# Optimization experiments

Measured on AMD Instinct MI355X. Metric: run time of the kernel, lower is better.

## Reference

```python
import jax, jax.numpy as jnp
import numpy as np

# Config mirrors init_kwargs
H_FULL, W_FULL = 360, 720
SCALE = 4
H_LO, W_LO = H_FULL // SCALE, W_FULL // SCALE  # 90, 180
LMAX = H_LO                  # 90
MMAX = W_LO // 2 + 1         # 91
C = 128                      # embed_dim
NL = 4                       # num_layers
INP_CH, OUT_CH = 2, 2
MLP_HID = int(C * 2.0)
EPS = 1e-5


def rfft2_trunc(x):
    # RealFFT2.forward: ortho rfft2, keep first ceil(LMAX/2) and last floor(LMAX/2) lat modes, first MMAX lon modes
    y = jnp.fft.rfft2(x, norm="ortho")
    lt = (LMAX + 1) // 2
    lb = LMAX - lt
    return jnp.concatenate([y[..., :lt, :MMAX], y[..., y.shape[-2] - lb:, :MMAX]], axis=-2)


def irfft2_pad(y, H, W):
    # InverseRealFFT2: zero-pad truncated modes back to full spectrum, ortho irfft2
    lt = (LMAX + 1) // 2
    lb = LMAX - lt
    full = jnp.zeros(y.shape[:-2] + (H, W // 2 + 1), dtype=y.dtype)
    full = full.at[..., :lt, :MMAX].set(y[..., :lt, :])
    full = full.at[..., H - lb:, :MMAX].set(y[..., lt:, :])
    return jnp.fft.irfft2(full, s=(H, W), norm="ortho")


def inorm(x, w, b):
    # InstanceNorm2d(affine=True): per-sample, per-channel over spatial dims, biased var
    mu = x.mean(axis=(-2, -1), keepdims=True)
    var = x.var(axis=(-2, -1), keepdims=True)
    xn = (x - mu) * jax.lax.rsqrt(var + EPS)
    return xn * w[None, :, None, None] + b[None, :, None, None]


def conv1x1(x, w):  # w: [Cout, Cin], bias=False
    return jnp.einsum('bihw,oi->bohw', x, w)


def gelu(x):
    return jax.nn.gelu(x, approximate=False)


def fno_block(x, n0w, n0b, swr, swi, iw, n1w, n1b, mw1, mw2, out_hw):
    in_hw = x.shape[-2:]
    xn = inorm(x, n0w, n0b)
    # SpectralConv (dhconv): complex per-l channel mixing in truncated spectral space
    Xc = rfft2_trunc(xn)                                   # [B,C,LMAX,MMAX] complex
    scale_res = tuple(in_hw) != tuple(out_hw)
    residual = irfft2_pad(Xc, out_hw[0], out_hw[1]) if scale_res else xn
    w = swr + 1j * swi                                      # [Cin,Cout,LMAX]
    Yc = jnp.einsum('bilm,iol->bolm', Xc, w)
    h = irfft2_pad(Yc, out_hw[0], out_hw[1])
    h = h + conv1x1(residual, iw)                           # inner linear skip
    h = gelu(h)                                             # act_layer0
    h = inorm(h, n1w, n1b)                                  # norm1
    h = conv1x1(gelu(conv1x1(h, mw1)), mw2)                 # MLP (1x1 convs)
    return h + residual                                     # outer identity skip


def setup_inputs() -> dict:
    key = jax.random.key(0)
    ks = jax.random.split(key, 16)
    s = 1.0 / np.sqrt(C)
    inp = {
        "x": jax.random.normal(ks[0], (1, INP_CH, H_FULL, W_FULL), jnp.float32),
        # encoder: inp_chans -> C -> C (encoder_ratio=1)
        "enc_w1": jax.random.normal(ks[1], (C, INP_CH), jnp.float32) * (1.0 / np.sqrt(INP_CH)),
        "enc_w2": jax.random.normal(ks[2], (C, C), jnp.float32) * s,
        # per-layer stacked block params
        "n0w": jnp.ones((NL, C), jnp.float32),
        "n0b": jnp.zeros((NL, C), jnp.float32),
        "swr": jax.random.normal(ks[3], (NL, C, C, LMAX), jnp.float32) * (1.0 / C),
        "swi": jax.random.normal(ks[4], (NL, C, C, LMAX), jnp.float32) * (1.0 / C),
        "iw": jax.random.normal(ks[5], (NL, C, C), jnp.float32) * s,
        "n1w": jnp.ones((NL, C), jnp.float32),
        "n1b": jnp.zeros((NL, C), jnp.float32),
        "mw1": jax.random.normal(ks[6], (NL, MLP_HID, C), jnp.float32) * s,
        "mw2": jax.random.normal(ks[7], (NL, C, MLP_HID), jnp.float32) * (1.0 / np.sqrt(MLP_HID)),
        # decoder: (C + inp_chans) -> C -> out_chans (big_skip concat)
        "dec_w1": jax.random.normal(ks[8], (C, C + INP_CH), jnp.float32) * (1.0 / np.sqrt(C + INP_CH)),
        "dec_w2": jax.random.normal(ks[9], (OUT_CH, C), jnp.float32) * s,
    }
    return inp


def reference(x, enc_w1, enc_w2, n0w, n0b, swr, swi, iw, n1w, n1b, mw1, mw2, dec_w1, dec_w2):
    big_res = x
    h = conv1x1(gelu(conv1x1(x, enc_w1)), enc_w2)           # encoder
    out_shapes = [(H_LO, W_LO)] * (NL - 1) + [(H_FULL, W_FULL)]
    for l in range(NL):
        h = fno_block(h, n0w[l], n0b[l], swr[l], swi[l], iw[l],
                      n1w[l], n1b[l], mw1[l], mw2[l], out_shapes[l])
    h = jnp.concatenate([h, big_res], axis=1)               # big skip
    h = conv1x1(gelu(conv1x1(h, dec_w1)), dec_w2)           # decoder
    return h
```

## Files before the change

### kernel.cpp

```cpp
#include <hip/hip_runtime.h>
#include <hip/hip_bf16.h>
#include <math.h>

typedef __attribute__((ext_vector_type(8))) short short8v;
typedef __attribute__((ext_vector_type(4))) float f32x4;
typedef unsigned short u16;

__device__ __forceinline__ float gelu_f(float x) {
    return 0.5f * x * (1.0f + erff(x * 0.70710678118654752f));
}
__device__ __forceinline__ float bf2f(u16 u) {
    union { unsigned int i; float f; } v; v.i = ((unsigned int)u) << 16; return v.f;
}
__device__ __forceinline__ u16 f2bf(float f) {
    union { float f; unsigned int i; } v; v.f = f;
    unsigned int r = v.i + 0x7FFFu + ((v.i >> 16) & 1u);
    return (u16)(r >> 16);
}

__device__ __forceinline__ uint4 load8(const u16* p) { return *(const uint4*)p; }
__device__ __forceinline__ uint4 load8(const float* p) {
    float4 a = *(const float4*)p;
    float4 b = *(const float4*)(p + 4);
    union { uint4 u; u16 e[8]; } r;
    r.e[0] = f2bf(a.x); r.e[1] = f2bf(a.y); r.e[2] = f2bf(a.z); r.e[3] = f2bf(a.w);
    r.e[4] = f2bf(b.x); r.e[5] = f2bf(b.y); r.e[6] = f2bf(b.z); r.e[7] = f2bf(b.w);
    return r.u;
}
__device__ __forceinline__ float rdD(const u16* p) { return bf2f(*p); }
__device__ __forceinline__ float rdD(const float* p) { return *p; }
__device__ __forceinline__ void stO(u16* p, float v) { *p = f2bf(v); }
__device__ __forceinline__ void stO(float* p, float v) { *p = v; }

template<int BMODE, class TA, class TB, class TD, class TO>
__global__ __launch_bounds__(256) void gemm_t(
    const TA* __restrict__ A1, const TB* __restrict__ B1,
    const TA* __restrict__ A2, const TB* __restrict__ B2,
    const TD* __restrict__ D, TO* __restrict__ O,
    int M, int N, int Kp, int neg2, int act,
    long long sAb, long long sAm,
    long long sBb, long long sBr,
    long long sDb, long long sDm,
    long long sOb, long long sOm)
{
    __shared__ __align__(16) u16 As[64 * 32];
    __shared__ __align__(16) u16 Bs[BMODE ? 32 * 68 : 64 * 32];
    const int tid = threadIdx.x;
    const long long b = blockIdx.z;
    const int bm0 = blockIdx.y * 64;
    const int bn0 = blockIdx.x * 64;
    const int lane = tid & 63;
    const int wave = tid >> 6;
    const int wr = (wave >> 1) * 32;
    const int wc = (wave & 1) * 32;
    const int fr = lane & 15;
    const int fg = lane >> 4;
    const int arow = tid >> 2, achk = tid & 3;

    f32x4 acc[2][2];
#pragma unroll
    for (int i = 0; i < 2; ++i)
#pragma unroll
        for (int j = 0; j < 2; ++j) acc[i][j] = (f32x4){0.f, 0.f, 0.f, 0.f};

    const int nph = A2 ? 2 : 1;
    for (int ph = 0; ph < nph; ++ph) {
        const TA* Ap = (ph ? A2 : A1) + b * sAb;
        const TB* Bp = (ph ? B2 : B1) + b * sBb;
        const unsigned int sgn = (ph && neg2) ? 0x80008000u : 0u;
        for (int k0 = 0; k0 < Kp; k0 += 32) {
            uint4 av = load8(Ap + (long long)(bm0 + arow) * sAm + k0 + achk * 8);
            av.x ^= sgn; av.y ^= sgn; av.z ^= sgn; av.w ^= sgn;
            uint4 bv;
            if (BMODE == 0) {
                bv = load8(Bp + (long long)(bn0 + arow) * sBr + k0 + achk * 8);
            } else {
                const int bk = tid >> 3, bnc = tid & 7;
                bv = load8(Bp + (long long)(k0 + bk) * sBr + bn0 + bnc * 8);
            }
            __syncthreads();
            *(uint4*)(&As[arow * 32 + ((achk ^ ((arow >> 1) & 3)) * 8)]) = av;
            if (BMODE == 0) {
                *(uint4*)(&Bs[arow * 32 + ((achk ^ ((arow >> 1) & 3)) * 8)]) = bv;
            } else {
                const int bk = tid >> 3, bnc = tid & 7;
                *(uint2*)(&Bs[bk * 68 + bnc * 8]) = make_uint2(bv.x, bv.y);
                *(uint2*)(&Bs[bk * 68 + bnc * 8 + 4]) = make_uint2(bv.z, bv.w);
            }
            __syncthreads();
            short8v afrag[2], bfrag[2];
#pragma unroll
            for (int i = 0; i < 2; ++i) {
                int r = wr + i * 16 + fr;
                afrag[i] = *(const short8v*)(&As[r * 32 + ((fg ^ ((r >> 1) & 3)) * 8)]);
            }
            if (BMODE == 0) {
#pragma unroll
                for (int j = 0; j < 2; ++j) {
                    int r = wc + j * 16 + fr;
                    bfrag[j] = *(const short8v*)(&Bs[r * 32 + ((fg ^ ((r >> 1) & 3)) * 8)]);
                }
            } else {
#pragma unroll
                for (int j = 0; j < 2; ++j) {
                    int col = wc + j * 16 + fr;
                    short8v v;
#pragma unroll
                    for (int e = 0; e < 8; ++e) v[e] = (short)Bs[(fg * 8 + e) * 68 + col];
                    bfrag[j] = v;
                }
            }
#pragma unroll
            for (int i = 0; i < 2; ++i)
#pragma unroll
                for (int j = 0; j < 2; ++j)
                    acc[i][j] = __builtin_amdgcn_mfma_f32_16x16x32_bf16(afrag[i], bfrag[j], acc[i][j], 0, 0, 0);
        }
    }
#pragma unroll
    for (int i = 0; i < 2; ++i) {
#pragma unroll
        for (int j = 0; j < 2; ++j) {
            int col = bn0 + wc + j * 16 + fr;
            if (col >= N) continue;
#pragma unroll
            for (int r = 0; r < 4; ++r) {
                int row = bm0 + wr + i * 16 + fg * 4 + r;
                if (row >= M) continue;
                float v = acc[i][j][r];
                if (D) v += rdD(D + b * sDb + (long long)row * sDm + col);
                if (act) v = gelu_f(v);
                stO(O + b * sOb + (long long)row * sOm + col, v);
            }
        }
    }
}

__global__ void gen_fwdW_T(u16* Cm, u16* Sm, int RP, int KP, int W, int MM) {
    int idx = blockIdx.x * blockDim.x + threadIdx.x;
    if (idx >= RP * KP) return;
    int m = idx / KP, w = idx % KP;
    float cv = 0.f, sv = 0.f;
    if (m < MM && w < W) {
        int t = (m * w) % W;
        float arg = 2.0f * (float)t / (float)W;
        float s = 1.0f / sqrtf((float)W);
        cv = cospif(arg) * s; sv = -sinpif(arg) * s;
    }
    Cm[idx] = f2bf(cv); Sm[idx] = f2bf(sv);
}
__global__ void gen_fwdH(u16* Cm, u16* Sm, int RP, int KP, int H) {
    int idx = blockIdx.x * blockDim.x + threadIdx.x;
    if (idx >= RP * KP) return;
    int l = idx / KP, h = idx % KP;
    float cv = 0.f, sv = 0.f;
    if (l < 90 && h < H) {
        int ll = (l < 45) ? l : l + H - 90;
        int t = (ll * h) % H;
        float arg = 2.0f * (float)t / (float)H;
        float s = 1.0f / sqrtf((float)H);
        cv = cospif(arg) * s; sv = sinpif(arg) * s;
    }
    Cm[idx] = f2bf(cv); Sm[idx] = f2bf(sv);
}
__global__ void gen_invH(u16* Cm, u16* Sm, int RP, int KP, int H) {
    int idx = blockIdx.x * blockDim.x + threadIdx.x;
    if (idx >= RP * KP) return;
    int y = idx / KP, l = idx % KP;
    float cv = 0.f, sv = 0.f;
    if (y < H && l < 90) {
        int ll = (l < 45) ? l : l + H - 90;
        int t = (ll * y) % H;
        float arg = 2.0f * (float)t / (float)H;
        float s = 1.0f / sqrtf((float)H);
        cv = cospif(arg) * s; sv = sinpif(arg) * s;
    }
    Cm[idx] = f2bf(cv); Sm[idx] = f2bf(sv);
}
__global__ void gen_invW_T(u16* Cm, u16* Sm, int RP, int KP, int W, int MM) {
    int idx = blockIdx.x * blockDim.x + threadIdx.x;
    if (idx >= RP * KP) return;
    int w = idx / KP, m = idx % KP;
    float cv = 0.f, sv = 0.f;
    if (w < W && m < MM) {
        int t = (m * w) % W;
        float arg = 2.0f * (float)t / (float)W;
        bool nyq = (2 * m == W);
        float wt = (m == 0 || nyq) ? 1.0f : 2.0f;
        float s = wt / sqrtf((float)W);
        cv = cospif(arg) * s;
        sv = nyq ? 0.f : sinpif(arg) * s;
    }
    Cm[idx] = f2bf(cv); Sm[idx] = f2bf(sv);
}

__global__ void w2bf(const float* __restrict__ in, u16* __restrict__ out, int R, int K, int rs) {
    int idx = blockIdx.x * blockDim.x + threadIdx.x;
    if (idx >= R * K) return;
    int r = idx / K, c = idx % K;
    out[idx] = f2bf(in[(long long)r * rs + c]);
}
__global__ void transp_sw(const float* __restrict__ in, u16* __restrict__ out) {
    __shared__ float t[32][33];
    int l0 = blockIdx.x * 32, ci0 = blockIdx.y * 32, co = blockIdx.z;
    int tx = threadIdx.x, ty = threadIdx.y;
#pragma unroll
    for (int rr = 0; rr < 4; ++rr) {
        int ci = ci0 + ty + rr * 8;
        int l = l0 + tx;
        t[ty + rr * 8][tx] = (l < 90) ? in[((long long)ci * 128 + co) * 90 + l] : 0.f;
    }
    __syncthreads();
#pragma unroll
    for (int rr = 0; rr < 4; ++rr) {
        int l = l0 + ty + rr * 8;
        int ci = ci0 + tx;
        if (l < 90) out[((long long)l * 128 + co) * 128 + ci] = f2bf(t[tx][ty + rr * 8]);
    }
}

__global__ __launch_bounds__(256) void stats_cl_bf(const u16* __restrict__ x, long long P,
                                                   float2* __restrict__ part, int nch) {
    int chunk = blockIdx.x;
    int c = threadIdx.x & 127;
    int h = threadIdx.x >> 7;
    long long beg = P * chunk / nch, end = P * (chunk + 1) / nch;
    float s = 0.f, q = 0.f;
    long long p = beg + h;
    for (; p + 14 < end; p += 16) {
        float v[8];
#pragma unroll
        for (int u = 0; u < 8; ++u) v[u] = bf2f(x[(p + 2 * u) * 128 + c]);
#pragma unroll
        for (int u = 0; u < 8; ++u) { s += v[u]; q += v[u] * v[u]; }
    }
    for (; p < end; p += 2) {
        float v = bf2f(x[p * 128 + c]);
        s += v; q += v * v;
    }
    __shared__ float rs[256], rq[256];
    rs[threadIdx.x] = s; rq[threadIdx.x] = q;
    __syncthreads();
    if (threadIdx.x < 128)
        part[(long long)c * nch + chunk] = make_float2(rs[c] + rs[c + 128], rq[c] + rq[c + 128]);
}
__global__ __launch_bounds__(256) void stats_cl_f32(const float* __restrict__ x, long long P,
                                                    float2* __restrict__ part, int nch) {
    int chunk = blockIdx.x;
    long long beg = P * chunk / nch, end = P * (chunk + 1) / nch;
    int c32 = threadIdx.x & 31;
    int pr  = threadIdx.x >> 5;
    float s[4], q[4];
#pragma unroll
    for (int k = 0; k < 4; ++k) { s[k] = 0.f; q[k] = 0.f; }
    for (long long p = beg + pr; p < end; p += 8) {
        float4 v = *(const float4*)(x + p * 128 + c32 * 4);
        float e[4] = {v.x, v.y, v.z, v.w};
#pragma unroll
        for (int k = 0; k < 4; ++k) { s[k] += e[k]; q[k] += e[k] * e[k]; }
    }
#pragma unroll
    for (int k = 0; k < 4; ++k) {
        s[k] += __shfl_xor(s[k], 32); q[k] += __shfl_xor(q[k], 32);
    }
    __shared__ float2 lds[4][128];
    int wv = threadIdx.x >> 6, lane = threadIdx.x & 63;
    if (lane < 32) {
#pragma unroll
        for (int k = 0; k < 4; ++k) lds[wv][lane * 4 + k] = make_float2(s[k], q[k]);
    }
    __syncthreads();
    if (threadIdx.x < 128) {
        float2 a = lds[0][threadIdx.x], b2 = lds[1][threadIdx.x];
        float2 c2 = lds[2][threadIdx.x], d2 = lds[3][threadIdx.x];
        part[(long long)threadIdx.x * nch + chunk] =
            make_float2(a.x + b2.x + c2.x + d2.x, a.y + b2.y + c2.y + d2.y);
    }
}
__global__ void stats_fin(const float2* __restrict__ part, int nch, float Pf,
                          const float* __restrict__ w, const float* __restrict__ b,
                          float2* __restrict__ st) {
    int c = threadIdx.x;
    float s = 0.f, q = 0.f;
    for (int i = 0; i < nch; ++i) { float2 p = part[(long long)c * nch + i]; s += p.x; q += p.y; }
    float mu = s / Pf;
    float var = q / Pf - mu * mu;
    float inv = rsqrtf(var + 1e-5f);
    float sc = w[c] * inv;
    st[c] = make_float2(sc, b[c] - mu * sc);
}
__global__ __launch_bounds__(256) void norm_apply_bf(const u16* __restrict__ src, u16* __restrict__ dst,
                                                     long long n8, const float2* __restrict__ st) {
    long long i = (long long)blockIdx.x * 256 + threadIdx.x;
    if (i >= n8) return;
    int c0 = (int)((i * 8) & 127);
    uint4 v = *(const uint4*)(src + i * 8);
    union { uint4 u; u16 e[8]; } in, out;
    in.u = v;
#pragma unroll
    for (int k = 0; k < 8; ++k) {
        float2 s = st[c0 + k];
        out.e[k] = f2bf(bf2f(in.e[k]) * s.x + s.y);
    }
    *(uint4*)(dst + i * 8) = out.u;
}
__global__ __launch_bounds__(256) void norm_apply_f32(const float4* __restrict__ src, float4* __restrict__ dst,
                                                      long long n4, const float2* __restrict__ st) {
    long long i = (long long)blockIdx.x * 256 + threadIdx.x;
    if (i >= n4) return;
    int c0 = (int)((i * 4) & 127);
    float4 v = src[i];
    float2 s0 = st[c0], s1 = st[c0 + 1], s2 = st[c0 + 2], s3 = st[c0 + 3];
    v.x = v.x * s0.x + s0.y;
    v.y = v.y * s1.x + s1.y;
    v.z = v.z * s2.x + s2.y;
    v.w = v.w * s3.x + s3.y;
    dst[i] = v;
}

__global__ __launch_bounds__(256) void enc_front(const float* __restrict__ x, const float* __restrict__ w1,
                                                 u16* __restrict__ out, long long P) {
    long long idx = (long long)blockIdx.x * 256 + threadIdx.x;
    if (idx >= P * 16) return;
    long long p = idx >> 4;
    int c0 = (int)(idx & 15) * 8;
    float x0 = x[p], x1 = x[P + p];
    union { uint4 u; u16 e[8]; } o;
#pragma unroll
    for (int k = 0; k < 8; ++k) {
        int c = c0 + k;
        o.e[k] = f2bf(gelu_f(w1[c * 2] * x0 + w1[c * 2 + 1] * x1));
    }
    *(uint4*)(out + p * 128 + c0) = o.u;
}
__global__ __launch_bounds__(256) void dec_mid(u16* __restrict__ s, const float* __restrict__ dw1,
                                               const float* __restrict__ x, long long P) {
    long long idx = (long long)blockIdx.x * 256 + threadIdx.x;
    if (idx >= P * 16) return;
    long long p = idx >> 4;
    int c0 = (int)(idx & 15) * 8;
    float x0 = x[p], x1 = x[P + p];
    union { uint4 u; u16 e[8]; } io;
    io.u = *(const uint4*)(s + p * 128 + c0);
#pragma unroll
    for (int k = 0; k < 8; ++k) {
        int c = c0 + k;
        io.e[k] = f2bf(gelu_f(bf2f(io.e[k]) + dw1[c * 130 + 128] * x0 + dw1[c * 130 + 129] * x1));
    }
    *(uint4*)(s + p * 128 + c0) = io.u;
}
__global__ __launch_bounds__(256) void dec_back(const u16* __restrict__ d1, const float* __restrict__ w2,
                                                float* __restrict__ out, long long P) {
    __shared__ float w2s[256];
    w2s[threadIdx.x] = w2[threadIdx.x];
    __syncthreads();
    int lane = threadIdx.x & 63;
    long long pix = (long long)blockIdx.x * 4 + (threadIdx.x >> 6);
    unsigned int pr = *(const unsigned int*)(d1 + pix * 128 + lane * 2);
    float b0 = bf2f((u16)(pr & 0xFFFF)), b1 = bf2f((u16)(pr >> 16));
    float s0 = b0 * w2s[lane * 2] + b1 * w2s[lane * 2 + 1];
    float s1 = b0 * w2s[128 + lane * 2] + b1 * w2s[128 + lane * 2 + 1];
#pragma unroll
    for (int off = 1; off < 64; off <<= 1) {
        s0 += __shfl_xor(s0, off);
        s1 += __shfl_xor(s1, off);
    }
    if (lane == 0) { out[pix] = s0; out[P + pix] = s1; }
}

__global__ void zero_out(float* p, long long n) {
    long long i = (long long)blockIdx.x * 256 + threadIdx.x;
    if (i < n) p[i] = 0.f;
}

extern "C" void kernel_launch(void* const* d_in, const int* in_sizes, int n_in,
                              void* d_out, int out_size, void* d_ws, size_t ws_size,
                              hipStream_t stream)
{
    const int HF = 360, WF = 720, HL = 90, WL = 180, C = 128, MM = 91;
    const long long PF = (long long)HF * WF;
    const long long PL = (long long)HL * WL;
    (void)in_sizes; (void)n_in;

    const float* x      = (const float*)d_in[0];
    const float* enc_w1 = (const float*)d_in[1];
    const float* enc_w2 = (const float*)d_in[2];
    const float* n0w    = (const float*)d_in[3];
    const float* n0b    = (const float*)d_in[4];
    const float* swr    = (const float*)d_in[5];
    const float* swi    = (const float*)d_in[6];
    const float* iw     = (const float*)d_in[7];
    const float* n1w    = (const float*)d_in[8];
    const float* n1b    = (const float*)d_in[9];
    const float* mw1    = (const float*)d_in[10];
    const float* mw2    = (const float*)d_in[11];
    const float* dec_w1 = (const float*)d_in[12];
    const float* dec_w2 = (const float*)d_in[13];
    float* outp = (float*)d_out;

    u16* ws = (u16*)d_ws;
    long long off = 0;
    auto alloc = [&](long long n) { u16* p = ws + off; off += (n + 31) & ~31LL; return p; };
    auto allocF = [&](long long n) { return (float*)alloc(2 * n); };

    u16*   FULL = alloc(PF * C);
    u16*   RES  = alloc(PF * C);
    u16*   S1r  = alloc(96LL * 384 * 128);
    u16*   S1i  = alloc(96LL * 384 * 128);
    float* Xr   = allocF(96LL * 96 * 128);
    float* Xi   = allocF(96LL * 96 * 128);
    float* Yr   = allocF(96LL * 96 * 128);
    float* Yi   = allocF(96LL * 96 * 128);
    u16*   G1r  = alloc(360LL * 96 * 128);
    u16*   G1i  = alloc(360LL * 96 * 128);
    u16*   G3r  = alloc(360LL * 96 * 128);
    u16*   G3i  = alloc(360LL * 96 * 128);
    float* Rlo  = allocF(PL * C);
    float* L0   = allocF(PL * C);
    u16*   HID  = alloc(43200LL * 256);
    u16*   WtR  = alloc(90LL * 128 * 128);
    u16*   WtI  = alloc(90LL * 128 * 128);
    u16* encw2b = alloc(128 * 128);
    u16* iwb    = alloc(128 * 128);
    u16* m1b    = alloc(256 * 128);
    u16* m2b    = alloc(128 * 256);
    u16* dw1b   = alloc(128 * 128);
    u16* CwTc_h = alloc(128 * 736); u16* CwTs_h = alloc(128 * 736);
    u16* CwTc_l = alloc(128 * 192); u16* CwTs_l = alloc(128 * 192);
    u16* Chc_h  = alloc(128 * 384); u16* Chs_h  = alloc(128 * 384);
    u16* Chc_l  = alloc(128 * 96);  u16* Chs_l  = alloc(128 * 96);
    u16* C2c_h  = alloc(384 * 96);  u16* C2s_h  = alloc(384 * 96);
    u16* C2c_l  = alloc(128 * 96);  u16* C2s_l  = alloc(128 * 96);
    u16* CwIc_h = alloc(768 * 96);  u16* CwIs_h = alloc(768 * 96);
    u16* CwIc_l = alloc(192 * 96);  u16* CwIs_l = alloc(192 * 96);
    float2* PART = (float2*)alloc(128 * 256 * 4);
    float2* STb  = (float2*)alloc(128 * 4);
    alloc(64 * 1024);

    if ((size_t)(off * 2) > ws_size) {
        zero_out<<<(int)((out_size + 255) / 256), 256, 0, stream>>>(outp, out_size);
        return;
    }

    auto grid3 = [](int M, int N, int batch) {
        return dim3((unsigned)((N + 63) / 64), (unsigned)((M + 63) / 64), (unsigned)batch);
    };
    auto inormB = [&](const u16* src, u16* dst, long long P, int nch,
                      const float* w, const float* b) {
        stats_cl_bf<<<nch, 256, 0, stream>>>(src, P, PART, nch);
        stats_fin<<<1, 128, 0, stream>>>(PART, nch, (float)P, w, b, STb);
        long long n8 = P * 128 / 8;
        norm_apply_bf<<<(int)((n8 + 255) / 256), 256, 0, stream>>>(src, dst, n8, STb);
    };
    auto inormF = [&](const float* src, float* dst, long long P, int nch,
                      const float* w, const float* b) {
        stats_cl_f32<<<nch, 256, 0, stream>>>(src, P, PART, nch);
        stats_fin<<<1, 128, 0, stream>>>(PART, nch, (float)P, w, b, STb);
        long long n4 = P * 128 / 4;
        norm_apply_f32<<<(int)((n4 + 255) / 256), 256, 0, stream>>>(
            (const float4*)src, (float4*)dst, n4, STb);
    };

    const u16* nullU = nullptr;
    const float* nullF = nullptr;

    {
        int n;
        n = 128 * 736; gen_fwdW_T<<<(n + 255) / 256, 256, 0, stream>>>(CwTc_h, CwTs_h, 128, 736, 720, MM);
        n = 128 * 192; gen_fwdW_T<<<(n + 255) / 256, 256, 0, stream>>>(CwTc_l, CwTs_l, 128, 192, 180, MM);
        n = 128 * 384; gen_fwdH<<<(n + 255) / 256, 256, 0, stream>>>(Chc_h, Chs_h, 128, 384, 360);
        n = 128 * 96;  gen_fwdH<<<(n + 255) / 256, 256, 0, stream>>>(Chc_l, Chs_l, 128, 96, 90);
        n = 384 * 96;  gen_invH<<<(n + 255) / 256, 256, 0, stream>>>(C2c_h, C2s_h, 384, 96, 360);
        n = 128 * 96;  gen_invH<<<(n + 255) / 256, 256, 0, stream>>>(C2c_l, C2s_l, 128, 96, 90);
        n = 768 * 96;  gen_invW_T<<<(n + 255) / 256, 256, 0, stream>>>(CwIc_h, CwIs_h, 768, 96, 720, MM);
        n = 192 * 96;  gen_invW_T<<<(n + 255) / 256, 256, 0, stream>>>(CwIc_l, CwIs_l, 192, 96, 180, MM);
        n = 128 * 128; w2bf<<<(n + 255) / 256, 256, 0, stream>>>(enc_w2, encw2b, 128, 128, 128);
        n = 128 * 128; w2bf<<<(n + 255) / 256, 256, 0, stream>>>(dec_w1, dw1b, 128, 128, 130);
    }

    enc_front<<<(int)((PF * 16 + 255) / 256), 256, 0, stream>>>(x, enc_w1, RES, PF);
    gemm_t<0, u16, u16, u16, u16><<<grid3((int)PF, 128, 1), 256, 0, stream>>>(
        RES, encw2b, nullU, nullU, nullU, FULL, (int)PF, 128, 128, 0, 0,
        0, 128, 0, 128, 0, 0, 0, 128);

    const long long s96 = 96LL * 128;

    for (int l = 0; l < 4; ++l) {
        const bool inHi = (l == 0), outHi = (l == 3);
        const int Hin = inHi ? HF : HL, Win = inHi ? WF : WL;
        const int Hout = outHi ? HF : HL, Wout = outHi ? WF : WL;
        const long long Pout = (long long)Hout * Wout;
        const int hdim = inHi ? 384 : 96;
        const int Wp = inHi ? 736 : 192;
        const int hp = inHi ? 384 : 96;
        const u16* CwTc = inHi ? CwTc_h : CwTc_l;  const u16* CwTs = inHi ? CwTs_h : CwTs_l;
        const u16* Chc  = inHi ? Chc_h  : Chc_l;   const u16* Chs  = inHi ? Chs_h  : Chs_l;
        const u16* C2c  = outHi ? C2c_h : C2c_l;   const u16* C2s  = outHi ? C2s_h : C2s_l;
        const u16* CwIc = outHi ? CwIc_h : CwIc_l; const u16* CwIs = outHi ? CwIs_h : CwIs_l;

        {
            dim3 gt(3, 4, 128); dim3 bt(32, 8);
            transp_sw<<<gt, bt, 0, stream>>>(swr + (long long)l * C * C * 90, WtR);
            transp_sw<<<gt, bt, 0, stream>>>(swi + (long long)l * C * C * 90, WtI);
            int n = 128 * 128; w2bf<<<(n + 255) / 256, 256, 0, stream>>>(iw + (long long)l * C * C, iwb, 128, 128, 128);
            n = 256 * 128; w2bf<<<(n + 255) / 256, 256, 0, stream>>>(mw1 + (long long)l * 256 * C, m1b, 256, 128, 128);
            n = 128 * 256; w2bf<<<(n + 255) / 256, 256, 0, stream>>>(mw2 + (long long)l * C * 256, m2b, 128, 256, 256);
        }

        if (inHi) {
            inormB(FULL, RES, PF, 256, n0w + l * C, n0b + l * C);
            gemm_t<1, u16, u16, u16, u16><<<grid3(96, 128, Hin), 256, 0, stream>>>(
                CwTc, RES, nullU, nullU, nullU, S1r, 96, 128, Wp, 0, 0,
                0, Wp, (long long)Win * 128, 128, 0, 0, 128, (long long)hdim * 128);
            gemm_t<1, u16, u16, u16, u16><<<grid3(96, 128, Hin), 256, 0, stream>>>(
                CwTs, RES, nullU, nullU, nullU, S1i, 96, 128, Wp, 0, 0,
                0, Wp, (long long)Win * 128, 128, 0, 0, 128, (long long)hdim * 128);
        } else {
            inormF(Rlo, L0, PL, 128, n0w + l * C, n0b + l * C);
            gemm_t<1, u16, float, u16, u16><<<grid3(96, 128, Hin), 256, 0, stream>>>(
                CwTc, L0, nullU, nullF, nullU, S1r, 96, 128, Wp, 0, 0,
                0, Wp, (long long)Win * 128, 128, 0, 0, 128, (long long)hdim * 128);
            gemm_t<1, u16, float, u16, u16><<<grid3(96, 128, Hin), 256, 0, stream>>>(
                CwTs, L0, nullU, nullF, nullU, S1i, 96, 128, Wp, 0, 0,
                0, Wp, (long long)Win * 128, 128, 0, 0, 128, (long long)hdim * 128);
        }

        gemm_t<1, u16, u16, u16, float><<<grid3(96, 128, 96), 256, 0, stream>>>(
            Chc, S1r, Chs, S1i, nullU, Xr, 96, 128, hp, 0, 0,
            0, hp, (long long)hdim * 128, 128, 0, 0, 128, s96);
        gemm_t<1, u16, u16, u16, float><<<grid3(96, 128, 96), 256, 0, stream>>>(
            Chc, S1i, Chs, S1r, nullU, Xi, 96, 128, hp, 1, 0,
            0, hp, (long long)hdim * 128, 128, 0, 0, 128, s96);

        if (inHi || outHi) {
            gemm_t<1, u16, float, u16, u16><<<grid3(Hout, 128, 96), 256, 0, stream>>>(
                C2c, Xr, C2s, Xi, nullU, G3r, Hout, 128, 96, 1, 0,
                0, 96, 128, s96, 0, 0, 128, s96);
            gemm_t<1, u16, float, u16, u16><<<grid3(Hout, 128, 96), 256, 0, stream>>>(
                C2c, Xi, C2s, Xr, nullU, G3i, Hout, 128, 96, 0, 0,
                0, 96, 128, s96, 0, 0, 128, s96);
        }

        gemm_t<0, float, u16, u16, float><<<grid3(96, 128, 90), 256, 0, stream>>>(
            Xr, WtR, Xi, WtI, nullU, Yr, 96, 128, 128, 1, 0,
            s96, 128, 128LL * 128, 128, 0, 0, 128, s96);
        gemm_t<0, float, u16, u16, float><<<grid3(96, 128, 90), 256, 0, stream>>>(
            Xr, WtI, Xi, WtR, nullU, Yi, 96, 128, 128, 0, 0,
            s96, 128, 128LL * 128, 128, 0, 0, 128, s96);

        gemm_t<1, u16, float, u16, u16><<<grid3(Hout, 128, 96), 256, 0, stream>>>(
            C2c, Yr, C2s, Yi, nullU, G1r, Hout, 128, 96, 1, 0,
            0, 96, s96, 128, 0, 0, 128, s96);
        gemm_t<1, u16, float, u16, u16><<<grid3(Hout, 128, 96), 256, 0, stream>>>(
            C2c, Yi, C2s, Yr, nullU, G1i, Hout, 128, 96, 0, 0,
            0, 96, s96, 128, 0, 0, 128, s96);

        if (!outHi) {
            gemm_t<1, u16, u16, u16, float><<<grid3(Wout, 128, Hout), 256, 0, stream>>>(
                CwIc, G1r, CwIs, G1i, nullU, Rlo, Wout, 128, 96, 1, 0,
                0, 96, s96, 128, 0, 0, (long long)Wout * 128, 128);
            if (inHi)
                gemm_t<1, u16, u16, u16, float><<<grid3(Wout, 128, Hout), 256, 0, stream>>>(
                    CwIc, G3r, CwIs, G3i, nullU, L0, Wout, 128, 96, 1, 0,
                    0, 96, s96, 128, 0, 0, (long long)Wout * 128, 128);
            gemm_t<0, float, u16, float, float><<<grid3((int)Pout, 128, 1), 256, 0, stream>>>(
                L0, iwb, nullF, nullU, Rlo, Rlo, (int)Pout, 128, 128, 0, 1,
                0, 128, 0, 128, 0, 128, 0, 128);
            inormF(Rlo, Rlo, Pout, 128, n1w + l * C, n1b + l * C);
            gemm_t<0, float, u16, u16, u16><<<grid3((int)Pout, 256, 1), 256, 0, stream>>>(
                Rlo, m1b, nullF, nullU, nullU, HID, (int)Pout, 256, 128, 0, 1,
                0, 128, 0, 128, 0, 0, 0, 256);
            gemm_t<0, u16, u16, float, float><<<grid3((int)Pout, 128, 1), 256, 0, stream>>>(
                HID, m2b, nullU, nullU, L0, Rlo, (int)Pout, 128, 256, 0, 0,
                0, 256, 0, 256, 0, 128, 0, 128);
        } else {
            gemm_t<1, u16, u16, u16, u16><<<grid3(Wout, 128, Hout), 256, 0, stream>>>(
                CwIc, G1r, CwIs, G1i, nullU, FULL, Wout, 128, 96, 1, 0,
                0, 96, s96, 128, 0, 0, (long long)Wout * 128, 128);
            gemm_t<1, u16, u16, u16, u16><<<grid3(Wout, 128, Hout), 256, 0, stream>>>(
                CwIc, G3r, CwIs, G3i, nullU, RES, Wout, 128, 96, 1, 0,
                0, 96, s96, 128, 0, 0, (long long)Wout * 128, 128);
            gemm_t<0, u16, u16, u16, u16><<<grid3((int)Pout, 128, 1), 256, 0, stream>>>(
                RES, iwb, nullU, nullU, FULL, FULL, (int)Pout, 128, 128, 0, 1,
                0, 128, 0, 128, 0, 128, 0, 128);
            inormB(FULL, FULL, Pout, 256, n1w + l * C, n1b + l * C);
            const int nchunk = 6;
            const long long chM = Pout / nchunk;
            for (int ch = 0; ch < nchunk; ++ch) {
                long long o2 = ch * chM * 128;
                gemm_t<0, u16, u16, u16, u16><<<grid3((int)chM, 256, 1), 256, 0, stream>>>(
                    FULL + o2, m1b, nullU, nullU, nullU, HID, (int)chM, 256, 128, 0, 1,
                    0, 128, 0, 128, 0, 0, 0, 256);
                gemm_t<0, u16, u16, u16, u16><<<grid3((int)chM, 128, 1), 256, 0, stream>>>(
                    HID, m2b, nullU, nullU, RES + o2, FULL + o2, (int)chM, 128, 256, 0, 0,
                    0, 256, 0, 256, 0, 128, 0, 128);
            }
        }
    }

    gemm_t<0, u16, u16, u16, u16><<<grid3((int)PF, 128, 1), 256, 0, stream>>>(
        FULL, dw1b, nullU, nullU, nullU, RES, (int)PF, 128, 128, 0, 0,
        0, 128, 0, 128, 0, 0, 0, 128);
    dec_mid<<<(int)((PF * 16 + 255) / 256), 256, 0, stream>>>(RES, dec_w1, x, PF);
    dec_back<<<(int)(PF / 4), 256, 0, stream>>>(RES, dec_w2, outp, PF);
}
```

Measured before the change: 1.440 ms.

## Fuse real/imaginary GEMM pairs into a single complex-GEMM kernel

Adds a gemm_t2 kernel that computes both output planes of a complex matrix product in one launch, loading the shared operand tiles once and applying sign flips by XOR on bf16 fragments. It replaces the paired real/imag launches for the forward DFT, the per-mode channel mixing and the inverse latitude DFT. The aim is to halve launches and global operand reads. In exchange each block holds twice the accumulators and more shared memory, which may lower occupancy.

```diff
diff --git a/kernel.cpp b/kernel.cpp
--- a/kernel.cpp
+++ b/kernel.cpp
@@ -16,6 +16,11 @@
     union { float f; unsigned int i; } v; v.f = f;
     unsigned int r = v.i + 0x7FFFu + ((v.i >> 16) & 1u);
     return (u16)(r >> 16);
+}
+__device__ __forceinline__ short8v negbf(short8v a) {
+    uint4 u = *(uint4*)&a;
+    u.x ^= 0x80008000u; u.y ^= 0x80008000u; u.z ^= 0x80008000u; u.w ^= 0x80008000u;
+    return *(short8v*)&u;
 }
 
 __device__ __forceinline__ uint4 load8(const u16* p) { return *(const uint4*)p; }
@@ -131,6 +136,151 @@
                 if (D) v += rdD(D + b * sDb + (long long)row * sDm + col);
                 if (act) v = gelu_f(v);
                 stO(O + b * sOb + (long long)row * sOm + col, v);
+            }
+        }
+    }
+}
+
+template<int BMODE, int MODE, class TA, class TB, class TO>
+__global__ __launch_bounds__(256) void gemm_t2(
+    const TA* __restrict__ A1, const TA* __restrict__ A2,
+    const TB* __restrict__ B1, const TB* __restrict__ B2,
+    TO* __restrict__ O1, TO* __restrict__ O2,
+    int M, int N, int Kp, int s2neg,
+    long long sAb, long long sAm,
+    long long sBb, long long sBr,
+    long long sOb, long long sOm)
+{
+    __shared__ __align__(16) u16 As1[64 * 32], As2[64 * 32];
+    __shared__ __align__(16) u16 Bs1[BMODE ? 32 * 68 : 64 * 32];
+    __shared__ __align__(16) u16 Bs2[(MODE == 1) ? 16 : (BMODE ? 32 * 68 : 64 * 32)];
+    const int tid = threadIdx.x;
+    const long long b = blockIdx.z;
+    const int bm0 = blockIdx.y * 64;
+    const int bn0 = blockIdx.x * 64;
+    const int lane = tid & 63;
+    const int wave = tid >> 6;
+    const int wr = (wave >> 1) * 32;
+    const int wc = (wave & 1) * 32;
+    const int fr = lane & 15;
+    const int fg = lane >> 4;
+    const int arow = tid >> 2, achk = tid & 3;
+    const int aswz = (achk ^ ((arow >> 1) & 3)) * 8;
+
+    f32x4 acc1[2][2], acc2[2][2];
+#pragma unroll
+    for (int i = 0; i < 2; ++i)
+#pragma unroll
+        for (int j = 0; j < 2; ++j) {
+            acc1[i][j] = (f32x4){0.f, 0.f, 0.f, 0.f};
+            acc2[i][j] = (f32x4){0.f, 0.f, 0.f, 0.f};
+        }
+
+    const TA* A1b = A1 + b * sAb;
+    const TA* A2b = A2 + b * sAb;
+    const TB* B1b = B1 + b * sBb;
+    const TB* B2b = (MODE == 0) ? B2 + b * sBb : B1;
+
+    for (int k0 = 0; k0 < Kp; k0 += 32) {
+        long long aoff = (long long)(bm0 + arow) * sAm + k0 + achk * 8;
+        uint4 av1 = load8(A1b + aoff);
+        uint4 av2 = load8(A2b + aoff);
+        uint4 bv1, bv2;
+        if (BMODE == 0) {
+            long long boff = (long long)(bn0 + arow) * sBr + k0 + achk * 8;
+            bv1 = load8(B1b + boff);
+            if (MODE == 0) bv2 = load8(B2b + boff);
+        } else {
+            const int bk = tid >> 3, bnc = tid & 7;
+            long long boff = (long long)(k0 + bk) * sBr + bn0 + bnc * 8;
+            bv1 = load8(B1b + boff);
+            if (MODE == 0) bv2 = load8(B2b + boff);
+        }
+        __syncthreads();
+        *(uint4*)(&As1[arow * 32 + aswz]) = av1;
+        *(uint4*)(&As2[arow * 32 + aswz]) = av2;
+        if (BMODE == 0) {
+            *(uint4*)(&Bs1[arow * 32 + aswz]) = bv1;
+            if (MODE == 0) *(uint4*)(&Bs2[arow * 32 + aswz]) = bv2;
+        } else {
+            const int bk = tid >> 3, bnc = tid & 7;
+            *(uint2*)(&Bs1[bk * 68 + bnc * 8]) = make_uint2(bv1.x, bv1.y);
+            *(uint2*)(&Bs1[bk * 68 + bnc * 8 + 4]) = make_uint2(bv1.z, bv1.w);
+            if (MODE == 0) {
+                *(uint2*)(&Bs2[bk * 68 + bnc * 8]) = make_uint2(bv2.x, bv2.y);
+                *(uint2*)(&Bs2[bk * 68 + bnc * 8 + 4]) = make_uint2(bv2.z, bv2.w);
+            }
+        }
+        __syncthreads();
+        short8v a1f[2], a2f[2], b1f[2], b2f[2];
+#pragma unroll
+        for (int i = 0; i < 2; ++i) {
+            int r = wr + i * 16 + fr;
+            int o = r * 32 + ((fg ^ ((r >> 1) & 3)) * 8);
+            a1f[i] = *(const short8v*)(&As1[o]);
+            a2f[i] = *(const short8v*)(&As2[o]);
+        }
+        if (BMODE == 0) {
+#pragma unroll
+            for (int j = 0; j < 2; ++j) {
+                int r = wc + j * 16 + fr;
+                int o = r * 32 + ((fg ^ ((r >> 1) & 3)) * 8);
+                b1f[j] = *(const short8v*)(&Bs1[o]);
+                if (MODE == 0) b2f[j] = *(const short8v*)(&Bs2[o]);
+            }
+        } else {
+#pragma unroll
+            for (int j = 0; j < 2; ++j) {
+                int col = wc + j * 16 + fr;
+                short8v v1, v2;
+#pragma unroll
+                for (int e = 0; e < 8; ++e) {
+                    v1[e] = (short)Bs1[(fg * 8 + e) * 68 + col];
+                    if (MODE == 0) v2[e] = (short)Bs2[(fg * 8 + e) * 68 + col];
+                }
+                b1f[j] = v1;
+                if (MODE == 0) b2f[j] = v2;
+            }
+        }
+        if (MODE == 1) {
+#pragma unroll
+            for (int i = 0; i < 2; ++i)
+#pragma unroll
+                for (int j = 0; j < 2; ++j) {
+                    acc1[i][j] = __builtin_amdgcn_mfma_f32_16x16x32_bf16(a1f[i], b1f[j], acc1[i][j], 0, 0, 0);
+                    acc2[i][j] = __builtin_amdgcn_mfma_f32_16x16x32_bf16(a2f[i], b1f[j], acc2[i][j], 0, 0, 0);
+                }
+        } else {
+            short8v a2p[2], a2m[2];
+#pragma unroll
+            for (int i = 0; i < 2; ++i) {
+                a2p[i] = s2neg ? negbf(a2f[i]) : a2f[i];
+                a2m[i] = s2neg ? a2f[i] : negbf(a2f[i]);
+            }
+#pragma unroll
+            for (int i = 0; i < 2; ++i)
+#pragma unroll
+                for (int j = 0; j < 2; ++j) {
+                    acc1[i][j] = __builtin_amdgcn_mfma_f32_16x16x32_bf16(a1f[i], b1f[j], acc1[i][j], 0, 0, 0);
+                    acc1[i][j] = __builtin_amdgcn_mfma_f32_16x16x32_bf16(a2p[i], b2f[j], acc1[i][j], 0, 0, 0);
+                    acc2[i][j] = __builtin_amdgcn_mfma_f32_16x16x32_bf16(a1f[i], b2f[j], acc2[i][j], 0, 0, 0);
+                    acc2[i][j] = __builtin_amdgcn_mfma_f32_16x16x32_bf16(a2m[i], b1f[j], acc2[i][j], 0, 0, 0);
+                }
+        }
+    }
+#pragma unroll
+    for (int i = 0; i < 2; ++i) {
+#pragma unroll
+        for (int j = 0; j < 2; ++j) {
+            int col = bn0 + wc + j * 16 + fr;
+            if (col >= N) continue;
+#pragma unroll
+            for (int r = 0; r < 4; ++r) {
+                int row = bm0 + wr + i * 16 + fg * 4 + r;
+                if (row >= M) continue;
+                long long oi = b * sOb + (long long)row * sOm + col;
+                stO(O1 + oi, acc1[i][j][r]);
+                stO(O2 + oi, acc2[i][j][r]);
             }
         }
     }
@@ -509,51 +659,33 @@
 
         if (inHi) {
             inormB(FULL, RES, PF, 256, n0w + l * C, n0b + l * C);
-            gemm_t<1, u16, u16, u16, u16><<<grid3(96, 128, Hin), 256, 0, stream>>>(
-                CwTc, RES, nullU, nullU, nullU, S1r, 96, 128, Wp, 0, 0,
-                0, Wp, (long long)Win * 128, 128, 0, 0, 128, (long long)hdim * 128);
-            gemm_t<1, u16, u16, u16, u16><<<grid3(96, 128, Hin), 256, 0, stream>>>(
-                CwTs, RES, nullU, nullU, nullU, S1i, 96, 128, Wp, 0, 0,
-                0, Wp, (long long)Win * 128, 128, 0, 0, 128, (long long)hdim * 128);
+            gemm_t2<1, 1, u16, u16, u16><<<grid3(96, 128, Hin), 256, 0, stream>>>(
+                CwTc, CwTs, RES, nullU, S1r, S1i, 96, 128, Wp, 0,
+                0, Wp, (long long)Win * 128, 128, 128, (long long)hdim * 128);
         } else {
             inormF(Rlo, L0, PL, 128, n0w + l * C, n0b + l * C);
-            gemm_t<1, u16, float, u16, u16><<<grid3(96, 128, Hin), 256, 0, stream>>>(
-                CwTc, L0, nullU, nullF, nullU, S1r, 96, 128, Wp, 0, 0,
-                0, Wp, (long long)Win * 128, 128, 0, 0, 128, (long long)hdim * 128);
-            gemm_t<1, u16, float, u16, u16><<<grid3(96, 128, Hin), 256, 0, stream>>>(
-                CwTs, L0, nullU, nullF, nullU, S1i, 96, 128, Wp, 0, 0,
-                0, Wp, (long long)Win * 128, 128, 0, 0, 128, (long long)hdim * 128);
-        }
-
-        gemm_t<1, u16, u16, u16, float><<<grid3(96, 128, 96), 256, 0, stream>>>(
-            Chc, S1r, Chs, S1i, nullU, Xr, 96, 128, hp, 0, 0,
-            0, hp, (long long)hdim * 128, 128, 0, 0, 128, s96);
-        gemm_t<1, u16, u16, u16, float><<<grid3(96, 128, 96), 256, 0, stream>>>(
-            Chc, S1i, Chs, S1r, nullU, Xi, 96, 128, hp, 1, 0,
-            0, hp, (long long)hdim * 128, 128, 0, 0, 128, s96);
+            gemm_t2<1, 1, u16, float, u16><<<grid3(96, 128, Hin), 256, 0, stream>>>(
+                CwTc, CwTs, L0, nullF, S1r, S1i, 96, 128, Wp, 0,
+                0, Wp, (long long)Win * 128, 128, 128, (long long)hdim * 128);
+        }
+
+        gemm_t2<1, 0, u16, u16, float><<<grid3(96, 128, 96), 256, 0, stream>>>(
+            Chc, Chs, S1r, S1i, Xr, Xi, 96, 128, hp, 0,
+            0, hp, (long long)hdim * 128, 128, 128, s96);
 
         if (inHi || outHi) {
-            gemm_t<1, u16, float, u16, u16><<<grid3(Hout, 128, 96), 256, 0, stream>>>(
-                C2c, Xr, C2s, Xi, nullU, G3r, Hout, 128, 96, 1, 0,
-                0, 96, 128, s96, 0, 0, 128, s96);
-            gemm_t<1, u16, float, u16, u16><<<grid3(Hout, 128, 96), 256, 0, stream>>>(
-                C2c, Xi, C2s, Xr, nullU, G3i, Hout, 128, 96, 0, 0,
-                0, 96, 128, s96, 0, 0, 128, s96);
-        }
-
-        gemm_t<0, float, u16, u16, float><<<grid3(96, 128, 90), 256, 0, stream>>>(
-            Xr, WtR, Xi, WtI, nullU, Yr, 96, 128, 128, 1, 0,
-            s96, 128, 128LL * 128, 128, 0, 0, 128, s96);
-        gemm_t<0, float, u16, u16, float><<<grid3(96, 128, 90), 256, 0, stream>>>(
-            Xr, WtI, Xi, WtR, nullU, Yi, 96, 128, 128, 0, 0,
-            s96, 128, 128LL * 128, 128, 0, 0, 128, s96);
-
-        gemm_t<1, u16, float, u16, u16><<<grid3(Hout, 128, 96), 256, 0, stream>>>(
-            C2c, Yr, C2s, Yi, nullU, G1r, Hout, 128, 96, 1, 0,
-            0, 96, s96, 128, 0, 0, 128, s96);
-        gemm_t<1, u16, float, u16, u16><<<grid3(Hout, 128, 96), 256, 0, stream>>>(
-            C2c, Yi, C2s, Yr, nullU, G1i, Hout, 128, 96, 0, 0,
-            0, 96, s96, 128, 0, 0, 128, s96);
+            gemm_t2<1, 0, u16, float, u16><<<grid3(Hout, 128, 96), 256, 0, stream>>>(
+                C2c, C2s, Xr, Xi, G3r, G3i, Hout, 128, 96, 1,
+                0, 96, 128, s96, 128, s96);
+        }
+
+        gemm_t2<0, 0, float, u16, float><<<grid3(96, 128, 90), 256, 0, stream>>>(
+            Xr, Xi, WtR, WtI, Yr, Yi, 96, 128, 128, 1,
+            s96, 128, 128LL * 128, 128, 128, s96);
+
+        gemm_t2<1, 0, u16, float, u16><<<grid3(Hout, 128, 96), 256, 0, stream>>>(
+            C2c, C2s, Yr, Yi, G1r, G1i, Hout, 128, 96, 1,
+            0, 96, s96, 128, 128, s96);
 
         if (!outHi) {
             gemm_t<1, u16, u16, u16, float><<<grid3(Wout, 128, Hout), 256, 0, stream>>>(
```

Result: faster. 1.294 ms (-10.1%).
